# Kernel optimization log

Hardware: AMD Instinct MI355X
Metric: run time of the kernel (lower is better)

Reference implementation:

```python
import jax, jax.numpy as jnp
import numpy as np

B, L, LC, C, CTX, H = 4, 2048, 512, 1024, 1024, 16
D = C // H
EPS = 1e-6
SCALE = 1.0 / np.float32(np.sqrt(D))


def _ln(x):
    # LayerNorm32, elementwise_affine applied outside when present
    mu = jnp.mean(x, axis=-1, keepdims=True)
    var = jnp.var(x, axis=-1, keepdims=True)
    return (x - mu) * jax.lax.rsqrt(var + EPS)


def _attn(q, k, v):
    # q: [B,Lq,H,D], k/v: [B,Lk,H,D] -> [B,Lq,C]
    s = jnp.einsum('bqhd,bkhd->bhqk', q, k) * SCALE
    p = jax.nn.softmax(s, axis=-1)
    o = jnp.einsum('bhqk,bkhd->bqhd', p, v)
    return o.reshape(o.shape[0], o.shape[1], C)


def setup_inputs() -> dict:
    key = jax.random.key(0)
    ks = jax.random.split(key, 12)
    s = 0.02
    w = lambda k, shape: (jax.random.normal(k, shape, jnp.float32) * s)
    z = lambda n: jnp.zeros((n,), jnp.float32)
    return {
        'x': jax.random.normal(ks[0], (B, L, C), jnp.float32),
        'mod': jax.random.normal(ks[1], (B, C), jnp.float32),
        'context': jax.random.normal(ks[2], (B, LC, CTX), jnp.float32),
        'w_ada': w(ks[3], (C, 6 * C)), 'b_ada': z(6 * C),
        'w_qkv': w(ks[4], (C, 3 * C)), 'b_qkv': z(3 * C),
        'w_so': w(ks[5], (C, C)), 'b_so': z(C),
        'g_n2': jnp.ones((C,), jnp.float32), 'b_n2': z(C),
        'w_cq': w(ks[6], (C, C)), 'b_cq': z(C),
        'w_ckv': w(ks[7], (CTX, 2 * C)), 'b_ckv': z(2 * C),
        'w_co': w(ks[8], (C, C)), 'b_co': z(C),
        'w_m1': w(ks[9], (C, 4 * C)), 'b_m1': z(4 * C),
        'w_m2': w(ks[10], (4 * C, C)), 'b_m2': z(C),
    }


def reference(x, mod, context, w_ada, b_ada, w_qkv, b_qkv, w_so, b_so,
              g_n2, b_n2, w_cq, b_cq, w_ckv, b_ckv, w_co, b_co,
              w_m1, b_m1, w_m2, b_m2):
    # adaLN modulation: SiLU -> Linear(C, 6C) -> chunk(6)
    ada = jax.nn.silu(mod) @ w_ada + b_ada  # [B, 6C]
    sh_msa, sc_msa, g_msa, sh_mlp, sc_mlp, g_mlp = jnp.split(ada, 6, axis=-1)
    ex = lambda t: t[:, None, :]  # broadcast per-sample over its token run

    # --- MSA branch ---
    h = _ln(x) * (1.0 + ex(sc_msa)) + ex(sh_msa)
    qkv = (h @ w_qkv + b_qkv).reshape(B, L, 3, H, D)
    h = _attn(qkv[:, :, 0], qkv[:, :, 1], qkv[:, :, 2]) @ w_so + b_so
    x = x + h * ex(g_msa)

    # --- MCA branch (norm2 has affine) ---
    h = _ln(x) * g_n2 + b_n2
    q = (h @ w_cq + b_cq).reshape(B, L, H, D)
    kv = (context @ w_ckv + b_ckv).reshape(B, LC, 2, H, D)
    h = _attn(q, kv[:, :, 0], kv[:, :, 1]) @ w_co + b_co
    x = x + h

    # --- FFN branch ---
    h = _ln(x) * (1.0 + ex(sc_mlp)) + ex(sh_mlp)
    h = jax.nn.gelu(h @ w_m1 + b_m1, approximate=False) @ w_m2 + b_m2
    x = x + h * ex(g_mlp)
    return x
```

## Files before the change

### kernel.cpp

```cpp
#include <hip/hip_runtime.h>
#include <cstdint>

typedef __bf16 bf16;
typedef __bf16 bf16x8 __attribute__((ext_vector_type(8)));
typedef __bf16 bf16x4 __attribute__((ext_vector_type(4)));
typedef float  floatx4 __attribute__((ext_vector_type(4)));
typedef unsigned int uint32x4 __attribute__((ext_vector_type(4)));

#define B_  4
#define L_  2048
#define LC_ 512
#define C_  1024
#define H_  16
#define D_  64

typedef const __attribute__((address_space(1))) unsigned int* as1_u32p;
typedef __attribute__((address_space(3))) unsigned int* as3_u32p;

__device__ __forceinline__ void async16(const void* g, void* l) {
  __builtin_amdgcn_global_load_lds((as1_u32p)g, (as3_u32p)l, 16, 0, 0);
}

__device__ __forceinline__ floatx4 mfma16(bf16x8 a, bf16x8 b, floatx4 c) {
  return __builtin_amdgcn_mfma_f32_16x16x32_bf16(a, b, c, 0, 0, 0);
}

__device__ __forceinline__ bool dt_bf16(const unsigned* dt) { return dt[0] == 0x3F803F80u; }

__device__ __forceinline__ float rd(const void* p, size_t i, bool bf) {
  return bf ? (float)((const bf16*)p)[i] : ((const float*)p)[i];
}

__global__ __launch_bounds__(256) void k_cvt(const void* __restrict__ src, bf16* __restrict__ dst,
                                             int N, const unsigned* __restrict__ dt) {
  bool bf = dt_bf16(dt);
  int i = (blockIdx.x * 256 + threadIdx.x) * 4;
  if (i + 3 < N) {
    for (int j = 0; j < 4; ++j) dst[i + j] = (bf16)rd(src, i + j, bf);
  } else {
    for (int j = 0; j < 4 && i + j < N; ++j) dst[i + j] = (bf16)rd(src, i + j, bf);
  }
}

struct CvtSrcs { const void* s[9]; };
__global__ __launch_bounds__(256) void k_cvt_all(CvtSrcs c, bf16* __restrict__ dst,
                                                 const unsigned* __restrict__ dt) {
  bool bf = dt_bf16(dt);
  int i = blockIdx.x * 256 + threadIdx.x;
  if (i >= 15360) return;
  const int pre[10] = {0, 3072, 4096, 5120, 6144, 7168, 9216, 10240, 14336, 15360};
  int seg = 0;
  #pragma unroll
  for (int k = 1; k < 9; ++k) if (i >= pre[k]) seg = k;
  dst[i] = (bf16)rd(c.s[seg], i - pre[seg], bf);
}

__global__ __launch_bounds__(256) void k_silu(const void* __restrict__ mod, float* __restrict__ sm,
                                              const unsigned* __restrict__ dt) {
  bool bf = dt_bf16(dt);
  int i = blockIdx.x * 256 + threadIdx.x;
  if (i < B_ * C_) {
    float v = rd(mod, i, bf);
    sm[i] = v / (1.f + __expf(-v));
  }
}

__global__ __launch_bounds__(256) void k_ada(const float* __restrict__ sm, const void* __restrict__ w,
                                             float* __restrict__ part, const unsigned* __restrict__ dt) {
  bool bf = dt_bf16(dt);
  int idx = blockIdx.x * 256 + threadIdx.x;
  int b = idx / 6144, j = idx - b * 6144;
  int k0 = blockIdx.y * 256;
  const float* s = sm + b * C_;
  float acc = 0.f;
  if (bf) {
    const bf16* W = (const bf16*)w;
    for (int k = k0; k < k0 + 256; ++k) acc += s[k] * (float)W[(size_t)k * 6144 + j];
  } else {
    const float* W = (const float*)w;
    for (int k = k0; k < k0 + 256; ++k) acc += s[k] * W[(size_t)k * 6144 + j];
  }
  part[(size_t)blockIdx.y * 24576 + idx] = acc;
}

__global__ __launch_bounds__(256) void k_ada_red(const float* __restrict__ part, const void* __restrict__ bv,
                                                 float* __restrict__ ada, const unsigned* __restrict__ dt) {
  bool bf = dt_bf16(dt);
  int idx = blockIdx.x * 256 + threadIdx.x;
  int j = idx % 6144;
  ada[idx] = rd(bv, j, bf) + part[idx] + part[24576 + idx] + part[49152 + idx] + part[73728 + idx];
}

struct TransDesc { const void* src; bf16* dst; int R, Cc, nCb, pre; };
struct TransDescs { TransDesc d[7]; };
__global__ __launch_bounds__(256) void k_trans_all(TransDescs t, const unsigned* __restrict__ dt) {
  bool bf = dt_bf16(dt);
  __shared__ bf16 tile[32][33];
  int blk = blockIdx.x;
  int di = 0;
  #pragma unroll
  for (int i = 1; i < 7; ++i) if (blk >= t.d[i].pre) di = i;
  const void* src = t.d[di].src;
  bf16* dst = t.d[di].dst;
  int R = t.d[di].R, Cc = t.d[di].Cc;
  int local = blk - t.d[di].pre;
  int bx = local % t.d[di].nCb, by = local / t.d[di].nCb;
  int c0 = bx * 32, r0 = by * 32;
  int tx = threadIdx.x & 31, ty = threadIdx.x >> 5;
  for (int i = 0; i < 4; ++i)
    tile[ty * 4 + i][tx] = (bf16)rd(src, (size_t)(r0 + ty * 4 + i) * Cc + c0 + tx, bf);
  __syncthreads();
  for (int i = 0; i < 4; ++i)
    dst[(size_t)(c0 + ty * 4 + i) * R + r0 + tx] = tile[tx][ty * 4 + i];
}

__global__ __launch_bounds__(256) void k_vt(const bf16* __restrict__ src, int ld, int off, int Lk,
                                            bf16* __restrict__ VT) {
  __shared__ bf16 tile[32][33];
  int l0 = blockIdx.x * 32;
  int d0 = blockIdx.y * 32;
  int bh = blockIdx.z, b = bh >> 4, h = bh & 15;
  int tx = threadIdx.x & 31, ty = threadIdx.x >> 5;
  for (int i = 0; i < 4; ++i) {
    int l = l0 + ty * 4 + i;
    tile[ty * 4 + i][tx] = src[((size_t)b * Lk + l) * ld + off + h * 64 + d0 + tx];
  }
  __syncthreads();
  for (int i = 0; i < 4; ++i) {
    int d = d0 + ty * 4 + i;
    VT[((size_t)bh * 64 + d) * Lk + l0 + tx] = tile[tx][ty * 4 + i];
  }
}

__global__ __launch_bounds__(256) void k_ln(const void* __restrict__ xraw, const float* __restrict__ xf,
                                            const unsigned* __restrict__ dt, bf16* __restrict__ out,
                                            const float* __restrict__ ada, int scOff, int shOff, float scAdd,
                                            const bf16* __restrict__ gcol, const bf16* __restrict__ bcol) {
  int row = blockIdx.x;
  int b = row >> 11;
  int base = row * C_ + threadIdx.x * 4;
  float v[4];
  if (xf) {
    for (int i = 0; i < 4; ++i) v[i] = xf[base + i];
  } else {
    bool bf = dt_bf16(dt);
    for (int i = 0; i < 4; ++i) v[i] = rd(xraw, base + i, bf);
  }
  float s1 = 0.f, s2 = 0.f;
  for (int i = 0; i < 4; ++i) { s1 += v[i]; s2 += v[i] * v[i]; }
  for (int m = 1; m < 64; m <<= 1) { s1 += __shfl_xor(s1, m); s2 += __shfl_xor(s2, m); }
  __shared__ float r1[4], r2[4];
  int w = threadIdx.x >> 6;
  if ((threadIdx.x & 63) == 0) { r1[w] = s1; r2[w] = s2; }
  __syncthreads();
  s1 = r1[0] + r1[1] + r1[2] + r1[3];
  s2 = r2[0] + r2[1] + r2[2] + r2[3];
  float mu = s1 * (1.f / (float)C_);
  float var = fmaxf(s2 * (1.f / (float)C_) - mu * mu, 0.f);
  float rstd = rsqrtf(var + 1e-6f);
  for (int i = 0; i < 4; ++i) {
    int c = threadIdx.x * 4 + i;
    float sc, sh;
    if (ada) { sc = scAdd + ada[b * 6144 + scOff + c]; sh = ada[b * 6144 + shOff + c]; }
    else     { sc = (float)gcol[c];                    sh = (float)bcol[c]; }
    out[base + i] = (bf16)((v[i] - mu) * rstd * sc + sh);
  }
}

template <int MODE>
__global__ __launch_bounds__(256) void k_gemm(const bf16* __restrict__ A, const bf16* __restrict__ Bt,
                                              const bf16* __restrict__ bias, void* __restrict__ outv,
                                              int M, int N, int K,
                                              const void* __restrict__ resid,
                                              const float* __restrict__ ada, int gateOff,
                                              const unsigned* __restrict__ dt,
                                              float qs, int qN) {
  __shared__ bf16 As[2 * 8192];
  __shared__ bf16 Bs[2 * 8192];
  const int tid = threadIdx.x;
  const int w = tid >> 6, lane = tid & 63;
  const int wr = w & 1, wc = w >> 1;
  const int g = lane >> 4, t = lane & 15;

  const int nbx = gridDim.x;
  const int nwg = nbx * gridDim.y;
  const int orig = blockIdx.y * nbx + blockIdx.x;
  const int qq = nwg >> 3, rrm = nwg & 7;
  const int xcd = orig & 7, sidx = orig >> 3;
  const int wgid = (xcd < rrm ? xcd * (qq + 1) : rrm * (qq + 1) + (xcd - rrm) * qq) + sidx;
  const int rowA0 = (wgid / nbx) * 128, rowB0 = (wgid % nbx) * 128;

  const bf16* Ag = A  + (size_t)(rowA0 + w * 32 + (lane >> 2)) * K + (lane & 3) * 8;
  const bf16* Bg = Bt + (size_t)(rowB0 + w * 32 + (lane >> 2)) * K + (lane & 3) * 8;

  auto stage = [&](int kb, int bufsel) {
    bf16* Ad = As + bufsel * 8192 + w * 1024;
    bf16* Bd = Bs + bufsel * 8192 + w * 1024;
    async16(Ag + kb,                       Ad);
    async16(Ag + kb + (size_t)16 * K,      Ad + 512);
    async16(Ag + kb + 32,                  Ad + 4096);
    async16(Ag + kb + 32 + (size_t)16 * K, Ad + 4096 + 512);
    async16(Bg + kb,                       Bd);
    async16(Bg + kb + (size_t)16 * K,      Bd + 512);
    async16(Bg + kb + 32,                  Bd + 4096);
    async16(Bg + kb + 32 + (size_t)16 * K, Bd + 4096 + 512);
  };

  floatx4 acc[4][4];
  for (int i = 0; i < 4; ++i) for (int j = 0; j < 4; ++j) for (int r = 0; r < 4; ++r) acc[i][j][r] = 0.f;

  stage(0, 0);
  __syncthreads();

  const int nkb = K >> 6;
  for (int it = 0; it < nkb; ++it) {
    const int cur = it & 1;
    if (it + 1 < nkb) stage((it + 1) << 6, cur ^ 1);
    const bf16* Asb = As + cur * 8192;
    const bf16* Bsb = Bs + cur * 8192;
    __builtin_amdgcn_s_setprio(1);
    #pragma unroll
    for (int kk = 0; kk < 2; ++kk) {
      bf16x8 af[4], bfr[4];
      #pragma unroll
      for (int mt = 0; mt < 4; ++mt) af[mt]  = *(const bf16x8*)&Asb[kk * 4096 + (wr * 64 + mt * 16 + t) * 32 + g * 8];
      #pragma unroll
      for (int nt = 0; nt < 4; ++nt) bfr[nt] = *(const bf16x8*)&Bsb[kk * 4096 + (wc * 64 + nt * 16 + t) * 32 + g * 8];
      #pragma unroll
      for (int mt = 0; mt < 4; ++mt)
        #pragma unroll
        for (int nt = 0; nt < 4; ++nt)
          acc[mt][nt] = mfma16(af[mt], bfr[nt], acc[mt][nt]);
    }
    __builtin_amdgcn_s_setprio(0);
    if (it + 1 < nkb) __syncthreads();
  }

  const bool bf = (MODE == 1 || MODE == 4) ? dt_bf16(dt) : false;
  for (int mt = 0; mt < 4; ++mt) {
    for (int nt = 0; nt < 4; ++nt) {
      int grow = rowA0 + wr * 64 + mt * 16 + g * 4;
      int gcol = rowB0 + wc * 64 + nt * 16 + t;
      float bvv = (float)bias[gcol];
      for (int r = 0; r < 4; ++r) {
        int rr = grow + r;
        float v = acc[mt][nt][r] + bvv;
        size_t idx = (size_t)rr * N + gcol;
        if (MODE == 0) {
          ((bf16*)outv)[idx] = (bf16)(v * ((gcol < qN) ? qs : 1.0f));
        } else if (MODE == 1) {
          float gt = ada[(rr >> 11) * 6144 + gateOff + gcol];
          ((float*)outv)[idx] = rd(resid, idx, bf) + v * gt;
        } else if (MODE == 2) {
          ((float*)outv)[idx] = ((const float*)resid)[idx] + v;
        } else if (MODE == 3) {
          ((bf16*)outv)[idx] = (bf16)(0.5f * v * (1.f + erff(v * 0.70710678118654752f)));
        } else {
          float gt = ada[(rr >> 11) * 6144 + gateOff + gcol];
          float val = ((const float*)resid)[idx] + v * gt;
          if (bf) ((bf16*)outv)[idx] = (bf16)val;
          else    ((float*)outv)[idx] = val;
        }
      }
    }
  }
}

__global__ __launch_bounds__(256) void k_attn(const bf16* __restrict__ Qb, int ldq, int qoff,
                                              const bf16* __restrict__ Kb, int ldk, int koff,
                                              const bf16* __restrict__ VT,
                                              bf16* __restrict__ Ob, int Lk) {
  __shared__ bf16 smem[20480];

  const int tid = threadIdx.x;
  const int w = tid >> 6, lane = tid & 63;
  const int g = lane >> 4, t = lane & 15;
  const int bh = blockIdx.y, b = bh >> 4, h = bh & 15;
  const int q0 = blockIdx.x * 64;

  const bf16* Q  = Qb + (size_t)(b * L_ + q0) * ldq + h * 64 + qoff;
  const bf16* K  = Kb + (size_t)b * Lk * ldk + h * 64 + koff;
  const bf16* Vt = VT + (size_t)bh * 64 * Lk;
  bf16* O = Ob + ((size_t)(b * L_ + q0 + w * 16 + t)) * C_ + h * 64;

  const int sr0 = w * 16 + (lane >> 3), sp = lane & 7;
  const int sr1 = sr0 + 8;
  const int sw0 = (sp ^ (sr0 & 7)) * 8;
  const int sw1 = (sp ^ (sr1 & 7)) * 8;

  bf16* Ps  = smem;
  bf16* KB0 = smem + 4096;
  bf16* VB0 = smem + 12288;

  async16(Q + (size_t)sr0 * ldq + sw0, smem + w * 1024);
  async16(Q + (size_t)sr1 * ldq + sw1, smem + w * 1024 + 512);
  async16(K + (size_t)sr0 * ldk + sw0, KB0 + w * 1024);
  async16(K + (size_t)sr1 * ldk + sw1, KB0 + w * 1024 + 512);
  async16(Vt + (size_t)sr0 * Lk + sw0, VB0 + w * 1024);
  async16(Vt + (size_t)sr1 * Lk + sw1, VB0 + w * 1024 + 512);
  __syncthreads();

  const int rowQ = w * 16 + t;
  bf16x8 bq[2];
  #pragma unroll
  for (int ko = 0; ko < 2; ++ko)
    bq[ko] = *(const bf16x8*)&smem[rowQ * 64 + (((ko * 4 + g) ^ (rowQ & 7)) * 8)];

  const int nt = Lk >> 6;

  if (nt > 1) {
    async16(K + (size_t)(64 + sr0) * ldk + sw0, KB0 + 4096 + w * 1024);
    async16(K + (size_t)(64 + sr1) * ldk + sw1, KB0 + 4096 + w * 1024 + 512);
  }

  floatx4 s[4];
  __builtin_amdgcn_s_setprio(1);
  #pragma unroll
  for (int mt = 0; mt < 4; ++mt) {
    floatx4 sa; for (int r = 0; r < 4; ++r) sa[r] = 0.f;
    #pragma unroll
    for (int ko = 0; ko < 2; ++ko) {
      int rowK = mt * 16 + t;
      bf16x8 ak = *(const bf16x8*)&KB0[rowK * 64 + (((ko * 4 + g) ^ (rowK & 7)) * 8)];
      sa = mfma16(ak, bq[ko], sa);
    }
    s[mt] = sa;
  }
  __builtin_amdgcn_s_setprio(0);
  __syncthreads();

  bf16x8 ones;
  #pragma unroll
  for (int i = 0; i < 8; ++i) ones[i] = (bf16)1.0f;

  floatx4 o_acc[4], o_sum;
  for (int d = 0; d < 4; ++d) for (int r = 0; r < 4; ++r) o_acc[d][r] = 0.f;
  for (int r = 0; r < 4; ++r) o_sum[r] = 0.f;

  const size_t kstep = (size_t)64 * ldk;
  const bf16* Kst0 = K + (size_t)(128 + sr0) * ldk + sw0;
  const bf16* Kst1 = K + (size_t)(128 + sr1) * ldk + sw1;
  const bf16* Vst0 = Vt + (size_t)sr0 * Lk + 64 + sw0;
  const bf16* Vst1 = Vt + (size_t)sr1 * Lk + 64 + sw1;

  for (int ti = 0; ti < nt; ++ti) {
    const int cur = ti & 1;

    if (ti + 2 < nt) {
      bf16* Kn = KB0 + cur * 4096 + w * 1024;
      async16(Kst0, Kn);
      async16(Kst1, Kn + 512);
    }
    if (ti + 1 < nt) {
      bf16* Vn = VB0 + ((ti + 1) & 1) * 4096 + w * 1024;
      async16(Vst0, Vn);
      async16(Vst1, Vn + 512);
    }
    Kst0 += kstep; Kst1 += kstep; Vst0 += 64; Vst1 += 64;

    float sv[16];
    #pragma unroll
    for (int mt = 0; mt < 4; ++mt)
      #pragma unroll
      for (int r = 0; r < 4; ++r) sv[mt * 4 + r] = exp2f(s[mt][r]);

    #pragma unroll
    for (int mt = 0; mt < 4; ++mt) {
      bf16x4 pk;
      for (int r = 0; r < 4; ++r) pk[r] = (bf16)sv[mt * 4 + r];
      int off = mt * 16 + g * 4;
      int chunk = off >> 3, sub = off & 7;
      *(bf16x4*)&Ps[rowQ * 64 + ((chunk ^ (rowQ & 7)) * 8) + sub] = pk;
    }

    if (ti + 1 < nt) {
      const bf16* Kc = KB0 + ((ti + 1) & 1) * 4096;
      __builtin_amdgcn_s_setprio(1);
      #pragma unroll
      for (int mt = 0; mt < 4; ++mt) {
        floatx4 sa; for (int r = 0; r < 4; ++r) sa[r] = 0.f;
        #pragma unroll
        for (int ko = 0; ko < 2; ++ko) {
          int rowK = mt * 16 + t;
          bf16x8 ak = *(const bf16x8*)&Kc[rowK * 64 + (((ko * 4 + g) ^ (rowK & 7)) * 8)];
          sa = mfma16(ak, bq[ko], sa);
        }
        s[mt] = sa;
      }
      __builtin_amdgcn_s_setprio(0);
    }

    const bf16* Vc = VB0 + cur * 4096;
    __builtin_amdgcn_s_setprio(1);
    #pragma unroll
    for (int ko = 0; ko < 2; ++ko) {
      bf16x8 bp = *(const bf16x8*)&Ps[rowQ * 64 + (((ko * 4 + g) ^ (rowQ & 7)) * 8)];
      o_sum = mfma16(ones, bp, o_sum);
      #pragma unroll
      for (int d = 0; d < 4; ++d) {
        int rowV = d * 16 + t;
        bf16x8 av = *(const bf16x8*)&Vc[rowV * 64 + (((ko * 4 + g) ^ (rowV & 7)) * 8)];
        o_acc[d] = mfma16(av, bp, o_acc[d]);
      }
    }
    __builtin_amdgcn_s_setprio(0);

    if (ti + 1 < nt) __syncthreads();
  }

  float rl = 1.f / o_sum[0];
  #pragma unroll
  for (int d = 0; d < 4; ++d) {
    bf16x4 ov;
    for (int r = 0; r < 4; ++r) ov[r] = (bf16)(o_acc[d][r] * rl);
    *(bf16x4*)&O[d * 16 + g * 4] = ov;
  }
}

extern "C" void kernel_launch(void* const* d_in, const int* in_sizes, int n_in,
                              void* d_out, int out_size, void* d_ws, size_t ws_size,
                              hipStream_t stream) {
  const void* x     = d_in[0];
  const void* mod   = d_in[1];
  const void* ctx   = d_in[2];
  const void* w_ada = d_in[3];
  const void* b_ada = d_in[4];
  const void* w_qkv = d_in[5];
  const void* b_qkv = d_in[6];
  const void* w_so  = d_in[7];
  const void* b_so  = d_in[8];
  const void* g_n2  = d_in[9];
  const void* b_n2  = d_in[10];
  const void* w_cq  = d_in[11];
  const void* b_cq  = d_in[12];
  const void* w_ckv = d_in[13];
  const void* b_ckv = d_in[14];
  const void* w_co  = d_in[15];
  const void* b_co  = d_in[16];
  const void* w_m1  = d_in[17];
  const void* b_m1  = d_in[18];
  const void* w_m2  = d_in[19];
  const void* b_m2  = d_in[20];
  const unsigned* dt = (const unsigned*)g_n2;

  char* p = (char*)d_ws;
  auto alloc = [&](size_t bytes) { char* r = p; p += (bytes + 255) & ~(size_t)255; return r; };
  float* sm    = (float*)alloc((size_t)B_ * C_ * 4);
  float* adp   = (float*)alloc((size_t)4 * 24576 * 4);
  float* ada   = (float*)alloc((size_t)B_ * 6144 * 4);
  bf16* wT_qkv = (bf16*)alloc((size_t)3072 * 1024 * 2);
  bf16* wT_so  = (bf16*)alloc((size_t)1024 * 1024 * 2);
  bf16* wT_cq  = (bf16*)alloc((size_t)1024 * 1024 * 2);
  bf16* wT_ckv = (bf16*)alloc((size_t)2048 * 1024 * 2);
  bf16* wT_co  = (bf16*)alloc((size_t)1024 * 1024 * 2);
  bf16* wT_m1  = (bf16*)alloc((size_t)4096 * 1024 * 2);
  bf16* wT_m2  = (bf16*)alloc((size_t)1024 * 4096 * 2);
  bf16* hb     = (bf16*)alloc((size_t)8192 * 1024 * 2);
  bf16* qkvb   = (bf16*)alloc((size_t)8192 * 3072 * 2);
  bf16* attn_o = (bf16*)alloc((size_t)8192 * 1024 * 2);
  float* xcur  = (float*)alloc((size_t)8192 * 1024 * 4);
  bf16* ctxb   = (bf16*)alloc((size_t)B_ * LC_ * 1024 * 2);
  bf16* biasb  = (bf16*)alloc(15360 * 2);
  bf16* bqkvb = biasb;
  bf16* bsob  = biasb + 3072;
  bf16* g2b   = biasb + 4096;
  bf16* b2b   = biasb + 5120;
  bf16* bcqb  = biasb + 6144;
  bf16* bckvb = biasb + 7168;
  bf16* bcob  = biasb + 9216;
  bf16* bm1b  = biasb + 10240;
  bf16* bm2b  = biasb + 14336;
  bf16* q2   = qkvb;
  bf16* kv   = qkvb + (size_t)8192 * 1024;
  bf16* gbuf = qkvb;
  bf16* vt   = hb;
  if (ws_size < (size_t)(p - (char*)d_ws)) return;

  dim3 blk(256);
  k_silu<<<16, blk, 0, stream>>>(mod, sm, dt);
  k_ada<<<dim3(96, 4), blk, 0, stream>>>(sm, w_ada, adp, dt);
  k_ada_red<<<96, blk, 0, stream>>>(adp, b_ada, ada, dt);
  k_cvt<<<2048, blk, 0, stream>>>(ctx, ctxb, B_ * LC_ * 1024, dt);
  CvtSrcs cs = {{b_qkv, b_so, g_n2, b_n2, b_cq, b_ckv, b_co, b_m1, b_m2}};
  k_cvt_all<<<60, blk, 0, stream>>>(cs, biasb, dt);
  TransDescs td = {{
    {w_qkv, wT_qkv, 1024, 3072,  96, 0},
    {w_so,  wT_so,  1024, 1024,  32, 3072},
    {w_cq,  wT_cq,  1024, 1024,  32, 4096},
    {w_ckv, wT_ckv, 1024, 2048,  64, 5120},
    {w_co,  wT_co,  1024, 1024,  32, 7168},
    {w_m1,  wT_m1,  1024, 4096, 128, 8192},
    {w_m2,  wT_m2,  4096, 1024,  32, 12288},
  }};
  k_trans_all<<<16384, blk, 0, stream>>>(td, dt);

  const float SC_L2E = 0.125f * 1.44269504088896f;

  k_ln<<<8192, blk, 0, stream>>>(x, nullptr, dt, hb, ada, 1024, 0, 1.0f, nullptr, nullptr);
  k_gemm<0><<<dim3(24, 64), blk, 0, stream>>>(hb, wT_qkv, bqkvb, qkvb, 8192, 3072, 1024, nullptr, nullptr, 0, dt, SC_L2E, 1024);
  k_vt<<<dim3(64, 2, 64), blk, 0, stream>>>(qkvb, 3072, 2048, L_, vt);
  k_attn<<<dim3(32, 64), blk, 0, stream>>>(qkvb, 3072, 0, qkvb, 3072, 1024, vt, attn_o, L_);
  k_gemm<1><<<dim3(8, 64), blk, 0, stream>>>(attn_o, wT_so, bsob, xcur, 8192, 1024, 1024, x, ada, 2048, dt, 1.f, 0);

  k_ln<<<8192, blk, 0, stream>>>(nullptr, xcur, dt, hb, nullptr, 0, 0, 0.f, g2b, b2b);
  k_gemm<0><<<dim3(8, 64), blk, 0, stream>>>(hb, wT_cq, bcqb, q2, 8192, 1024, 1024, nullptr, nullptr, 0, dt, SC_L2E, 1024);
  k_gemm<0><<<dim3(16, 16), blk, 0, stream>>>(ctxb, wT_ckv, bckvb, kv, 2048, 2048, 1024, nullptr, nullptr, 0, dt, 1.f, 0);
  k_vt<<<dim3(16, 2, 64), blk, 0, stream>>>(kv, 2048, 1024, LC_, vt);
  k_attn<<<dim3(32, 64), blk, 0, stream>>>(q2, 1024, 0, kv, 2048, 0, vt, attn_o, LC_);
  k_gemm<2><<<dim3(8, 64), blk, 0, stream>>>(attn_o, wT_co, bcob, xcur, 8192, 1024, 1024, xcur, nullptr, 0, dt, 1.f, 0);

  k_ln<<<8192, blk, 0, stream>>>(nullptr, xcur, dt, hb, ada, 4096, 3072, 1.0f, nullptr, nullptr);
  k_gemm<3><<<dim3(32, 64), blk, 0, stream>>>(hb, wT_m1, bm1b, gbuf, 8192, 4096, 1024, nullptr, nullptr, 0, dt, 1.f, 0);
  k_gemm<4><<<dim3(8, 64), blk, 0, stream>>>(gbuf, wT_m2, bm2b, d_out, 8192, 1024, 4096, xcur, ada, 5120, dt, 1.f, 0);
}
```

Measured before the change: 825.5 us.

## Add 256x128 triple-buffered swizzled GEMM with 8 waves for large projections

Adds a new GEMM kernel with 512 threads that computes a 256x128 output tile. It uses a three-stage LDS ring with XOR-swizzled 64-wide K rows, manual vmcnt waits and split A/B staging, so loads overlap compute and LDS bank conflicts drop. All large projection GEMMs except the context KV one switch to it. The old kernel stays only for the context KV projection, trimmed to the plain-store mode. The larger tile raises data reuse and the deeper pipeline hides memory latency, at the cost of about 144 KB of LDS per block (one block per CU) and fewer blocks in the grid.

After: 842.7 us. +2.1%, slower.

```diff
diff --git a/kernel.cpp b/kernel.cpp
--- a/kernel.cpp
+++ b/kernel.cpp
@@ -168,18 +168,17 @@
 }
 
 template <int MODE>
-__global__ __launch_bounds__(256) void k_gemm(const bf16* __restrict__ A, const bf16* __restrict__ Bt,
-                                              const bf16* __restrict__ bias, void* __restrict__ outv,
-                                              int M, int N, int K,
-                                              const void* __restrict__ resid,
-                                              const float* __restrict__ ada, int gateOff,
-                                              const unsigned* __restrict__ dt,
-                                              float qs, int qN) {
-  __shared__ bf16 As[2 * 8192];
-  __shared__ bf16 Bs[2 * 8192];
+__global__ __launch_bounds__(512) void k_gemm2(const bf16* __restrict__ A, const bf16* __restrict__ Bt,
+                                               const bf16* __restrict__ bias, void* __restrict__ outv,
+                                               int M, int N, int K,
+                                               const void* __restrict__ resid,
+                                               const float* __restrict__ ada, int gateOff,
+                                               const unsigned* __restrict__ dt,
+                                               float qs, int qN) {
+  __shared__ bf16 lds2[3 * 24576];
   const int tid = threadIdx.x;
-  const int w = tid >> 6, lane = tid & 63;
-  const int wr = w & 1, wc = w >> 1;
+  const int wid = tid >> 6, lane = tid & 63;
+  const int wr = wid & 3, wc = wid >> 2;
   const int g = lane >> 4, t = lane & 15;
 
   const int nbx = gridDim.x;
@@ -188,59 +187,93 @@
   const int qq = nwg >> 3, rrm = nwg & 7;
   const int xcd = orig & 7, sidx = orig >> 3;
   const int wgid = (xcd < rrm ? xcd * (qq + 1) : rrm * (qq + 1) + (xcd - rrm) * qq) + sidx;
-  const int rowA0 = (wgid / nbx) * 128, rowB0 = (wgid % nbx) * 128;
-
-  const bf16* Ag = A  + (size_t)(rowA0 + w * 32 + (lane >> 2)) * K + (lane & 3) * 8;
-  const bf16* Bg = Bt + (size_t)(rowB0 + w * 32 + (lane >> 2)) * K + (lane & 3) * 8;
-
-  auto stage = [&](int kb, int bufsel) {
-    bf16* Ad = As + bufsel * 8192 + w * 1024;
-    bf16* Bd = Bs + bufsel * 8192 + w * 1024;
-    async16(Ag + kb,                       Ad);
-    async16(Ag + kb + (size_t)16 * K,      Ad + 512);
-    async16(Ag + kb + 32,                  Ad + 4096);
-    async16(Ag + kb + 32 + (size_t)16 * K, Ad + 4096 + 512);
-    async16(Bg + kb,                       Bd);
-    async16(Bg + kb + (size_t)16 * K,      Bd + 512);
-    async16(Bg + kb + 32,                  Bd + 4096);
-    async16(Bg + kb + 32 + (size_t)16 * K, Bd + 4096 + 512);
+  const int rowA0b = (wgid / nbx) * 256;
+  const int rowB0b = (wgid % nbx) * 128;
+
+  const int srow = tid >> 3;
+  const int schunk = tid & 7;
+
+  auto stA = [&](bf16* buf, int kb) {
+    #pragma unroll
+    for (int l = 0; l < 4; ++l) {
+      int row = l * 64 + srow;
+      int srccol = ((schunk ^ (row & 7)) * 8);
+      async16(A + (size_t)(rowA0b + row) * K + kb + srccol, buf + row * 64 + schunk * 8);
+    }
+  };
+  auto stB = [&](bf16* buf, int kb) {
+    #pragma unroll
+    for (int l = 0; l < 2; ++l) {
+      int row = l * 64 + srow;
+      int srccol = ((schunk ^ (row & 7)) * 8);
+      async16(Bt + (size_t)(rowB0b + row) * K + kb + srccol, buf + 16384 + row * 64 + schunk * 8);
+    }
   };
 
   floatx4 acc[4][4];
   for (int i = 0; i < 4; ++i) for (int j = 0; j < 4; ++j) for (int r = 0; r < 4; ++r) acc[i][j][r] = 0.f;
 
-  stage(0, 0);
-  __syncthreads();
-
   const int nkb = K >> 6;
-  for (int it = 0; it < nkb; ++it) {
-    const int cur = it & 1;
-    if (it + 1 < nkb) stage((it + 1) << 6, cur ^ 1);
-    const bf16* Asb = As + cur * 8192;
-    const bf16* Bsb = Bs + cur * 8192;
-    __builtin_amdgcn_s_setprio(1);
-    #pragma unroll
-    for (int kk = 0; kk < 2; ++kk) {
+  stA(lds2, 0);             stB(lds2, 0);
+  stA(lds2 + 24576, 64);    stB(lds2 + 24576, 64);
+
+  int bcur = 0, bstg = 2;
+  int kbs = 128;
+  for (int T = 0; T < nkb; ++T) {
+    bf16* sb = lds2 + bstg * 24576;
+    const bool st2 = (T + 2 < nkb);
+    if (st2) stA(sb, kbs);
+    if (st2)                 { asm volatile("s_waitcnt vmcnt(10)" ::: "memory"); }
+    else if (T + 1 < nkb)    { asm volatile("s_waitcnt vmcnt(6)"  ::: "memory"); }
+    else                     { asm volatile("s_waitcnt vmcnt(0)"  ::: "memory"); }
+    __builtin_amdgcn_s_barrier();
+
+    const bf16* Ab = lds2 + bcur * 24576;
+    const bf16* Bb = Ab + 16384;
+    {
+      const int swz = ((0 * 4 + g) ^ (t & 7)) * 8;
       bf16x8 af[4], bfr[4];
       #pragma unroll
-      for (int mt = 0; mt < 4; ++mt) af[mt]  = *(const bf16x8*)&Asb[kk * 4096 + (wr * 64 + mt * 16 + t) * 32 + g * 8];
-      #pragma unroll
-      for (int nt = 0; nt < 4; ++nt) bfr[nt] = *(const bf16x8*)&Bsb[kk * 4096 + (wc * 64 + nt * 16 + t) * 32 + g * 8];
+      for (int mt = 0; mt < 4; ++mt) af[mt]  = *(const bf16x8*)&Ab[(wr * 64 + mt * 16 + t) * 64 + swz];
+      #pragma unroll
+      for (int nt = 0; nt < 4; ++nt) bfr[nt] = *(const bf16x8*)&Bb[(wc * 64 + nt * 16 + t) * 64 + swz];
+      __builtin_amdgcn_s_setprio(1);
       #pragma unroll
       for (int mt = 0; mt < 4; ++mt)
         #pragma unroll
         for (int nt = 0; nt < 4; ++nt)
           acc[mt][nt] = mfma16(af[mt], bfr[nt], acc[mt][nt]);
-    }
-    __builtin_amdgcn_s_setprio(0);
-    if (it + 1 < nkb) __syncthreads();
+      __builtin_amdgcn_s_setprio(0);
+    }
+    __builtin_amdgcn_s_barrier();
+    if (st2) stB(sb, kbs);
+    {
+      const int swz = ((1 * 4 + g) ^ (t & 7)) * 8;
+      bf16x8 af[4], bfr[4];
+      #pragma unroll
+      for (int mt = 0; mt < 4; ++mt) af[mt]  = *(const bf16x8*)&Ab[(wr * 64 + mt * 16 + t) * 64 + swz];
+      #pragma unroll
+      for (int nt = 0; nt < 4; ++nt) bfr[nt] = *(const bf16x8*)&Bb[(wc * 64 + nt * 16 + t) * 64 + swz];
+      __builtin_amdgcn_s_setprio(1);
+      #pragma unroll
+      for (int mt = 0; mt < 4; ++mt)
+        #pragma unroll
+        for (int nt = 0; nt < 4; ++nt)
+          acc[mt][nt] = mfma16(af[mt], bfr[nt], acc[mt][nt]);
+      __builtin_amdgcn_s_setprio(0);
+    }
+    __builtin_amdgcn_s_barrier();
+
+    bcur = (bcur == 2) ? 0 : bcur + 1;
+    bstg = (bstg == 2) ? 0 : bstg + 1;
+    kbs += 64;
   }
 
   const bool bf = (MODE == 1 || MODE == 4) ? dt_bf16(dt) : false;
   for (int mt = 0; mt < 4; ++mt) {
     for (int nt = 0; nt < 4; ++nt) {
-      int grow = rowA0 + wr * 64 + mt * 16 + g * 4;
-      int gcol = rowB0 + wc * 64 + nt * 16 + t;
+      int grow = rowA0b + wr * 64 + mt * 16 + g * 4;
+      int gcol = rowB0b + wc * 64 + nt * 16 + t;
       float bvv = (float)bias[gcol];
       for (int r = 0; r < 4; ++r) {
         int rr = grow + r;
@@ -260,6 +293,92 @@
           float val = ((const float*)resid)[idx] + v * gt;
           if (bf) ((bf16*)outv)[idx] = (bf16)val;
           else    ((float*)outv)[idx] = val;
+        }
+      }
+    }
+  }
+}
+
+template <int MODE>
+__global__ __launch_bounds__(256) void k_gemm(const bf16* __restrict__ A, const bf16* __restrict__ Bt,
+                                              const bf16* __restrict__ bias, void* __restrict__ outv,
+                                              int M, int N, int K,
+                                              const void* __restrict__ resid,
+                                              const float* __restrict__ ada, int gateOff,
+                                              const unsigned* __restrict__ dt,
+                                              float qs, int qN) {
+  __shared__ bf16 As[2 * 8192];
+  __shared__ bf16 Bs[2 * 8192];
+  const int tid = threadIdx.x;
+  const int w = tid >> 6, lane = tid & 63;
+  const int wr = w & 1, wc = w >> 1;
+  const int g = lane >> 4, t = lane & 15;
+
+  const int nbx = gridDim.x;
+  const int nwg = nbx * gridDim.y;
+  const int orig = blockIdx.y * nbx + blockIdx.x;
+  const int qq = nwg >> 3, rrm = nwg & 7;
+  const int xcd = orig & 7, sidx = orig >> 3;
+  const int wgid = (xcd < rrm ? xcd * (qq + 1) : rrm * (qq + 1) + (xcd - rrm) * qq) + sidx;
+  const int rowA0 = (wgid / nbx) * 128, rowB0 = (wgid % nbx) * 128;
+
+  const bf16* Ag = A  + (size_t)(rowA0 + w * 32 + (lane >> 2)) * K + (lane & 3) * 8;
+  const bf16* Bg = Bt + (size_t)(rowB0 + w * 32 + (lane >> 2)) * K + (lane & 3) * 8;
+
+  auto stage = [&](int kb, int bufsel) {
+    bf16* Ad = As + bufsel * 8192 + w * 1024;
+    bf16* Bd = Bs + bufsel * 8192 + w * 1024;
+    async16(Ag + kb,                       Ad);
+    async16(Ag + kb + (size_t)16 * K,      Ad + 512);
+    async16(Ag + kb + 32,                  Ad + 4096);
+    async16(Ag + kb + 32 + (size_t)16 * K, Ad + 4096 + 512);
+    async16(Bg + kb,                       Bd);
+    async16(Bg + kb + (size_t)16 * K,      Bd + 512);
+    async16(Bg + kb + 32,                  Bd + 4096);
+    async16(Bg + kb + 32 + (size_t)16 * K, Bd + 4096 + 512);
+  };
+
+  floatx4 acc[4][4];
+  for (int i = 0; i < 4; ++i) for (int j = 0; j < 4; ++j) for (int r = 0; r < 4; ++r) acc[i][j][r] = 0.f;
+
+  stage(0, 0);
+  __syncthreads();
+
+  const int nkb = K >> 6;
+  for (int it = 0; it < nkb; ++it) {
+    const int cur = it & 1;
+    if (it + 1 < nkb) stage((it + 1) << 6, cur ^ 1);
+    const bf16* Asb = As + cur * 8192;
+    const bf16* Bsb = Bs + cur * 8192;
+    __builtin_amdgcn_s_setprio(1);
+    #pragma unroll
+    for (int kk = 0; kk < 2; ++kk) {
+      bf16x8 af[4], bfr[4];
+      #pragma unroll
+      for (int mt = 0; mt < 4; ++mt) af[mt]  = *(const bf16x8*)&Asb[kk * 4096 + (wr * 64 + mt * 16 + t) * 32 + g * 8];
+      #pragma unroll
+      for (int nt = 0; nt < 4; ++nt) bfr[nt] = *(const bf16x8*)&Bsb[kk * 4096 + (wc * 64 + nt * 16 + t) * 32 + g * 8];
+      #pragma unroll
+      for (int mt = 0; mt < 4; ++mt)
+        #pragma unroll
+        for (int nt = 0; nt < 4; ++nt)
+          acc[mt][nt] = mfma16(af[mt], bfr[nt], acc[mt][nt]);
+    }
+    __builtin_amdgcn_s_setprio(0);
+    if (it + 1 < nkb) __syncthreads();
+  }
+
+  for (int mt = 0; mt < 4; ++mt) {
+    for (int nt = 0; nt < 4; ++nt) {
+      int grow = rowA0 + wr * 64 + mt * 16 + g * 4;
+      int gcol = rowB0 + wc * 64 + nt * 16 + t;
+      float bvv = (float)bias[gcol];
+      for (int r = 0; r < 4; ++r) {
+        int rr = grow + r;
+        float v = acc[mt][nt][r] + bvv;
+        size_t idx = (size_t)rr * N + gcol;
+        if (MODE == 0) {
+          ((bf16*)outv)[idx] = (bf16)(v * ((gcol < qN) ? qs : 1.0f));
         }
       }
     }
@@ -477,6 +596,7 @@
   if (ws_size < (size_t)(p - (char*)d_ws)) return;
 
   dim3 blk(256);
+  dim3 blk2(512);
   k_silu<<<16, blk, 0, stream>>>(mod, sm, dt);
   k_ada<<<dim3(96, 4), blk, 0, stream>>>(sm, w_ada, adp, dt);
   k_ada_red<<<96, blk, 0, stream>>>(adp, b_ada, ada, dt);
@@ -497,19 +617,19 @@
   const float SC_L2E = 0.125f * 1.44269504088896f;
 
   k_ln<<<8192, blk, 0, stream>>>(x, nullptr, dt, hb, ada, 1024, 0, 1.0f, nullptr, nullptr);
-  k_gemm<0><<<dim3(24, 64), blk, 0, stream>>>(hb, wT_qkv, bqkvb, qkvb, 8192, 3072, 1024, nullptr, nullptr, 0, dt, SC_L2E, 1024);
+  k_gemm2<0><<<dim3(24, 32), blk2, 0, stream>>>(hb, wT_qkv, bqkvb, qkvb, 8192, 3072, 1024, nullptr, nullptr, 0, dt, SC_L2E, 1024);
   k_vt<<<dim3(64, 2, 64), blk, 0, stream>>>(qkvb, 3072, 2048, L_, vt);
   k_attn<<<dim3(32, 64), blk, 0, stream>>>(qkvb, 3072, 0, qkvb, 3072, 1024, vt, attn_o, L_);
-  k_gemm<1><<<dim3(8, 64), blk, 0, stream>>>(attn_o, wT_so, bsob, xcur, 8192, 1024, 1024, x, ada, 2048, dt, 1.f, 0);
+  k_gemm2<1><<<dim3(8, 32), blk2, 0, stream>>>(attn_o, wT_so, bsob, xcur, 8192, 1024, 1024, x, ada, 2048, dt, 1.f, 0);
 
   k_ln<<<8192, blk, 0, stream>>>(nullptr, xcur, dt, hb, nullptr, 0, 0, 0.f, g2b, b2b);
-  k_gemm<0><<<dim3(8, 64), blk, 0, stream>>>(hb, wT_cq, bcqb, q2, 8192, 1024, 1024, nullptr, nullptr, 0, dt, SC_L2E, 1024);
+  k_gemm2<0><<<dim3(8, 32), blk2, 0, stream>>>(hb, wT_cq, bcqb, q2, 8192, 1024, 1024, nullptr, nullptr, 0, dt, SC_L2E, 1024);
   k_gemm<0><<<dim3(16, 16), blk, 0, stream>>>(ctxb, wT_ckv, bckvb, kv, 2048, 2048, 1024, nullptr, nullptr, 0, dt, 1.f, 0);
   k_vt<<<dim3(16, 2, 64), blk, 0, stream>>>(kv, 2048, 1024, LC_, vt);
   k_attn<<<dim3(32, 64), blk, 0, stream>>>(q2, 1024, 0, kv, 2048, 0, vt, attn_o, LC_);
-  k_gemm<2><<<dim3(8, 64), blk, 0, stream>>>(attn_o, wT_co, bcob, xcur, 8192, 1024, 1024, xcur, nullptr, 0, dt, 1.f, 0);
+  k_gemm2<2><<<dim3(8, 32), blk2, 0, stream>>>(attn_o, wT_co, bcob, xcur, 8192, 1024, 1024, xcur, nullptr, 0, dt, 1.f, 0);
 
   k_ln<<<8192, blk, 0, stream>>>(nullptr, xcur, dt, hb, ada, 4096, 3072, 1.0f, nullptr, nullptr);
-  k_gemm<3><<<dim3(32, 64), blk, 0, stream>>>(hb, wT_m1, bm1b, gbuf, 8192, 4096, 1024, nullptr, nullptr, 0, dt, 1.f, 0);
-  k_gemm<4><<<dim3(8, 64), blk, 0, stream>>>(gbuf, wT_m2, bm2b, d_out, 8192, 1024, 4096, xcur, ada, 5120, dt, 1.f, 0);
-}
+  k_gemm2<3><<<dim3(32, 32), blk2, 0, stream>>>(hb, wT_m1, bm1b, gbuf, 8192, 4096, 1024, nullptr, nullptr, 0, dt, 1.f, 0);
+  k_gemm2<4><<<dim3(8, 32), blk2, 0, stream>>>(gbuf, wT_m2, bm2b, d_out, 8192, 1024, 4096, xcur, ada, 5120, dt, 1.f, 0);
+}
```

## Split GEMM tile staging into A/B halves with fine-grained vmcnt waits

Applied to the files above, without the earlier changes.

Splits the async global-to-LDS staging of the next K-block into separate A and B issues, placing the B loads between the two k-substeps. It replaces __syncthreads with explicit s_waitcnt vmcnt/lgkmcnt plus s_barrier, so the wait holds only for the current tile's loads while the next tile's loads stay in flight. The goal is better overlap of global loads with MFMA work inside the GEMM main loop. The risk is a correctness hazard if the vmcnt counts or buffer reuse are wrong, since B of the next buffer is written while the other half is still being read.

New measurement: 899.4 us. +9.0%, slower.

```diff
diff --git a/kernel.cpp b/kernel.cpp
--- a/kernel.cpp
+++ b/kernel.cpp
@@ -193,13 +193,15 @@
   const bf16* Ag = A  + (size_t)(rowA0 + w * 32 + (lane >> 2)) * K + (lane & 3) * 8;
   const bf16* Bg = Bt + (size_t)(rowB0 + w * 32 + (lane >> 2)) * K + (lane & 3) * 8;
 
-  auto stage = [&](int kb, int bufsel) {
+  auto stageA = [&](int kb, int bufsel) {
     bf16* Ad = As + bufsel * 8192 + w * 1024;
-    bf16* Bd = Bs + bufsel * 8192 + w * 1024;
     async16(Ag + kb,                       Ad);
     async16(Ag + kb + (size_t)16 * K,      Ad + 512);
     async16(Ag + kb + 32,                  Ad + 4096);
     async16(Ag + kb + 32 + (size_t)16 * K, Ad + 4096 + 512);
+  };
+  auto stageB = [&](int kb, int bufsel) {
+    bf16* Bd = Bs + bufsel * 8192 + w * 1024;
     async16(Bg + kb,                       Bd);
     async16(Bg + kb + (size_t)16 * K,      Bd + 512);
     async16(Bg + kb + 32,                  Bd + 4096);
@@ -209,31 +211,54 @@
   floatx4 acc[4][4];
   for (int i = 0; i < 4; ++i) for (int j = 0; j < 4; ++j) for (int r = 0; r < 4; ++r) acc[i][j][r] = 0.f;
 
-  stage(0, 0);
-  __syncthreads();
+  stageA(0, 0);
+  stageB(0, 0);
 
   const int nkb = K >> 6;
   for (int it = 0; it < nkb; ++it) {
     const int cur = it & 1;
-    if (it + 1 < nkb) stage((it + 1) << 6, cur ^ 1);
+    const bool nx = (it + 1 < nkb);
+    if (nx) {
+      stageA((it + 1) << 6, cur ^ 1);
+      asm volatile("s_waitcnt vmcnt(4) lgkmcnt(0)" ::: "memory");
+    } else {
+      asm volatile("s_waitcnt vmcnt(0) lgkmcnt(0)" ::: "memory");
+    }
+    __builtin_amdgcn_s_barrier();
+
     const bf16* Asb = As + cur * 8192;
     const bf16* Bsb = Bs + cur * 8192;
-    __builtin_amdgcn_s_setprio(1);
-    #pragma unroll
-    for (int kk = 0; kk < 2; ++kk) {
+    {
       bf16x8 af[4], bfr[4];
       #pragma unroll
-      for (int mt = 0; mt < 4; ++mt) af[mt]  = *(const bf16x8*)&Asb[kk * 4096 + (wr * 64 + mt * 16 + t) * 32 + g * 8];
-      #pragma unroll
-      for (int nt = 0; nt < 4; ++nt) bfr[nt] = *(const bf16x8*)&Bsb[kk * 4096 + (wc * 64 + nt * 16 + t) * 32 + g * 8];
+      for (int mt = 0; mt < 4; ++mt) af[mt]  = *(const bf16x8*)&Asb[(wr * 64 + mt * 16 + t) * 32 + g * 8];
+      #pragma unroll
+      for (int nt = 0; nt < 4; ++nt) bfr[nt] = *(const bf16x8*)&Bsb[(wc * 64 + nt * 16 + t) * 32 + g * 8];
+      __builtin_amdgcn_s_setprio(1);
       #pragma unroll
       for (int mt = 0; mt < 4; ++mt)
         #pragma unroll
         for (int nt = 0; nt < 4; ++nt)
           acc[mt][nt] = mfma16(af[mt], bfr[nt], acc[mt][nt]);
-    }
-    __builtin_amdgcn_s_setprio(0);
-    if (it + 1 < nkb) __syncthreads();
+      __builtin_amdgcn_s_setprio(0);
+    }
+    if (nx) stageB((it + 1) << 6, cur ^ 1);
+    {
+      bf16x8 af[4], bfr[4];
+      #pragma unroll
+      for (int mt = 0; mt < 4; ++mt) af[mt]  = *(const bf16x8*)&Asb[4096 + (wr * 64 + mt * 16 + t) * 32 + g * 8];
+      #pragma unroll
+      for (int nt = 0; nt < 4; ++nt) bfr[nt] = *(const bf16x8*)&Bsb[4096 + (wc * 64 + nt * 16 + t) * 32 + g * 8];
+      __builtin_amdgcn_s_setprio(1);
+      #pragma unroll
+      for (int mt = 0; mt < 4; ++mt)
+        #pragma unroll
+        for (int nt = 0; nt < 4; ++nt)
+          acc[mt][nt] = mfma16(af[mt], bfr[nt], acc[mt][nt]);
+      __builtin_amdgcn_s_setprio(0);
+    }
+    asm volatile("s_waitcnt lgkmcnt(0)" ::: "memory");
+    __builtin_amdgcn_s_barrier();
   }
 
   const bool bf = (MODE == 1 || MODE == 4) ? dt_bf16(dt) : false;
```
